# Optimization experiments

Measured on AMD Instinct MI355X. Metric: run time of the kernel, lower is better.

Reference implementation:

```python
import jax, jax.numpy as jnp
import numpy as np

N = 6144
HIDDEN = 48
HEADS = 3
HEAD = HIDDEN // HEADS


def setup_inputs() -> dict:
    key = jax.random.key(0)
    ks = jax.random.split(key, 8)
    s = 1.0 / np.sqrt(HIDDEN)
    A = (jax.random.uniform(ks[0], (N, N)) < 0.05).astype(jnp.float32)
    h = jax.random.normal(ks[1], (N, HIDDEN), dtype=jnp.float32)
    Wq = jax.random.normal(ks[2], (HIDDEN, HIDDEN), dtype=jnp.float32) * s
    Wk = jax.random.normal(ks[3], (HIDDEN, HIDDEN), dtype=jnp.float32) * s
    Wv = jax.random.normal(ks[4], (HIDDEN, HIDDEN), dtype=jnp.float32) * s
    bq = jnp.zeros((HIDDEN,), jnp.float32)
    bk = jnp.zeros((HIDDEN,), jnp.float32)
    bv = jnp.zeros((HIDDEN,), jnp.float32)
    return {"A": A, "h": h, "Wq": Wq, "bq": bq, "Wk": Wk, "bk": bk, "Wv": Wv, "bv": bv}


def reference(A, h, Wq, bq, Wk, bk, Wv, bv):
    n = h.shape[0]
    # QKV projections (torch Linear: x @ W.T + b)
    q = (h @ Wq.T + bq).reshape(n, HEADS, HEAD).transpose(1, 0, 2)  # [H,N,d]
    k = (h @ Wk.T + bk).reshape(n, HEADS, HEAD).transpose(1, 0, 2)
    v = (h @ Wv.T + bv).reshape(n, HEADS, HEAD).transpose(1, 0, 2)
    # scores = (q k^T) * A / N**(-0.5)  == (q k^T) * A * sqrt(N)  (faithful to source)
    scale = jnp.asarray(n, h.dtype) ** 0.5
    scores = jnp.einsum("hnd,hmd->hnm", q, k) * A[None, :, :] * scale
    scores = jax.nn.softmax(scores, axis=2)
    out = jnp.einsum("hnm,hmd->hnd", scores, v)  # [H,N,d]
    out = out.transpose(1, 0, 2).reshape(n, HIDDEN)
    return (out, scores)
```

## Files before the change

### kernel.cpp

```cpp
#include <hip/hip_runtime.h>
#include <math.h>

#define NN   6144
#define HID  48
#define BLK  512
#define RPB  4
#define CAP  448
#define CTOT (RPB*CAP)
#define NSL  42
#define SCALE 78.38367176906175f

typedef float vf4 __attribute__((ext_vector_type(4)));

__global__ __launch_bounds__(256)
void qkv_kernel(const float* __restrict__ h,
                const float* __restrict__ Wq, const float* __restrict__ bq,
                const float* __restrict__ Wk, const float* __restrict__ bk,
                const float* __restrict__ Wv, const float* __restrict__ bv,
                float* __restrict__ qw, float* __restrict__ kw, float* __restrict__ vw) {
    int idx = blockIdx.x * blockDim.x + threadIdx.x;
    int i = idx / HID, c = idx % HID;
    const float4* h4  = (const float4*)(h + (size_t)i * HID);
    const float4* wq4 = (const float4*)(Wq + (size_t)c * HID);
    const float4* wk4 = (const float4*)(Wk + (size_t)c * HID);
    const float4* wv4 = (const float4*)(Wv + (size_t)c * HID);
    float aq = 0.f, ak = 0.f, av = 0.f;
    #pragma unroll
    for (int r = 0; r < HID / 4; ++r) {
        float4 hv = h4[r];
        float4 q4 = wq4[r], k4 = wk4[r], v4 = wv4[r];
        aq = fmaf(hv.x, q4.x, aq); aq = fmaf(hv.y, q4.y, aq);
        aq = fmaf(hv.z, q4.z, aq); aq = fmaf(hv.w, q4.w, aq);
        ak = fmaf(hv.x, k4.x, ak); ak = fmaf(hv.y, k4.y, ak);
        ak = fmaf(hv.z, k4.z, ak); ak = fmaf(hv.w, k4.w, ak);
        av = fmaf(hv.x, v4.x, av); av = fmaf(hv.y, v4.y, av);
        av = fmaf(hv.w, v4.w, av); av = fmaf(hv.z, v4.z, av);
    }
    aq += bq[c]; ak += bk[c]; av += bv[c];
    int head = c >> 4, d = c & 15;
    size_t off = ((size_t)head * NN + i) * 16 + d;
    qw[off] = aq; kw[off] = ak; vw[off] = av;
}

__global__ __launch_bounds__(256)
void vtot_kernel(const float* __restrict__ vw, float* __restrict__ vtot) {
    int c = blockIdx.x;
    int head = c >> 4, d = c & 15;
    float s = 0.f;
    for (int j = threadIdx.x; j < NN; j += 256)
        s += vw[((size_t)head * NN + j) * 16 + d];
    #pragma unroll
    for (int o = 32; o; o >>= 1) s += __shfl_xor(s, o, 64);
    __shared__ float red[4];
    int wid = threadIdx.x >> 6, lane = threadIdx.x & 63;
    if (lane == 0) red[wid] = s;
    __syncthreads();
    if (threadIdx.x == 0) vtot[c] = red[0] + red[1] + red[2] + red[3];
}

__device__ __forceinline__ float maxw(const float* w, int idx) {
    float m = 0.f;
    #pragma unroll
    for (int k = 0; k < 8; ++k) m = fmaxf(m, w[k * 12 + idx]);
    return m;
}

__global__ __launch_bounds__(BLK)
void attn_kernel(const float* __restrict__ A,
                 const float* __restrict__ qw, const float* __restrict__ kw,
                 const float* __restrict__ vw, const float* __restrict__ vtot,
                 float* __restrict__ out) {
    __shared__ int   list[CTOT];
    __shared__ float sc[3][CTOT];
    __shared__ __align__(16) float qs[RPB * 48];
    __shared__ float accL[RPB * 52];
    __shared__ float lAcc[12];
    __shared__ float wredM[8 * 12];
    __shared__ unsigned wlo[8], whi[8];

    const int i0 = blockIdx.x * RPB;
    const int tid = threadIdx.x;
    const int wid = tid >> 6, lane = tid & 63;

    if (tid < RPB * 48) {
        int r = tid / 48, c = tid % 48;
        int hh = c >> 4, d = c & 15;
        qs[tid] = qw[((size_t)hh * NN + (i0 + r)) * 16 + d];
    }
    if (tid < RPB * 52) accL[tid] = 0.f;
    if (tid < 12) lAcc[tid] = 0.f;

    unsigned long long amask = 0ull;
    #pragma unroll
    for (int r = 0; r < RPB; ++r) {
        const vf4* Ar = (const vf4*)(A + (size_t)(i0 + r) * NN);
        #pragma unroll
        for (int c = 0; c < 3; ++c) {
            vf4 a4 = __builtin_nontemporal_load(&Ar[tid + c * BLK]);
            int p = r * 16 + c * 4;
            if (a4.x != 0.f) amask |= 1ull << (p + 0);
            if (a4.y != 0.f) amask |= 1ull << (p + 1);
            if (a4.z != 0.f) amask |= 1ull << (p + 2);
            if (a4.w != 0.f) amask |= 1ull << (p + 3);
        }
    }
    unsigned m0 = (unsigned)(amask & 0xFFFull);
    unsigned m1 = (unsigned)((amask >> 16) & 0xFFFull);
    unsigned m2 = (unsigned)((amask >> 32) & 0xFFFull);
    unsigned m3 = (unsigned)((amask >> 48) & 0xFFFull);
    unsigned lo = (unsigned)__popc(m0) | ((unsigned)__popc(m1) << 16);
    unsigned hi = (unsigned)__popc(m2) | ((unsigned)__popc(m3) << 16);

    unsigned ilo = lo, ihi = hi;
    #pragma unroll
    for (int o = 1; o < 64; o <<= 1) {
        unsigned plo = __shfl_up(ilo, o, 64);
        unsigned phi = __shfl_up(ihi, o, 64);
        if (lane >= o) { ilo += plo; ihi += phi; }
    }
    if (lane == 63) { wlo[wid] = ilo; whi[wid] = ihi; }
    __syncthreads();
    unsigned blo = ilo - lo, bhi = ihi - hi;
    unsigned tlo = 0, thi = 0;
    #pragma unroll
    for (int w = 0; w < 8; ++w) {
        unsigned a = wlo[w], b = whi[w];
        if (w < wid) { blo += a; bhi += b; }
        tlo += a; thi += b;
    }
    const int C0 = min((int)(tlo & 0xFFFFu), CAP), C1 = min((int)(tlo >> 16), CAP);
    const int C2 = min((int)(thi & 0xFFFFu), CAP), C3 = min((int)(thi >> 16), CAP);
    const int cum1 = C0, cum2 = C0 + C1, cum3 = cum2 + C2;
    int bs[4] = {(int)(blo & 0xFFFFu), (int)(blo >> 16),
                 (int)(bhi & 0xFFFFu), (int)(bhi >> 16)};
    int cu[5] = {0, cum1, cum2, cum3, cum3 + C3};
    unsigned mr[4] = {m0, m1, m2, m3};
    int Cr4[4] = {C0, C1, C2, C3};

    #pragma unroll
    for (int r = 0; r < RPB; ++r) {
        unsigned m = mr[r];
        int b = bs[r];
        while (m) {
            int p = __ffs(m) - 1; m &= m - 1;
            if (b < CAP) list[cu[r] + b] = 4 * (tid + (p >> 2) * BLK) + (p & 3);
            ++b;
        }
    }
    __syncthreads();

    {
        const int q4 = tid >> 2, part = tid & 3;
        #pragma unroll
        for (int r = 0; r < RPB; ++r) {
            float4 qv0 = ((const float4*)(qs + r * 48 +  0))[part];
            float4 qv1 = ((const float4*)(qs + r * 48 + 16))[part];
            float4 qv2 = ((const float4*)(qs + r * 48 + 32))[part];
            float mx0 = 0.f, mx1 = 0.f, mx2 = 0.f;
            for (int e = cu[r] + q4; e < cu[r + 1]; e += (BLK >> 2)) {
                int j = list[e];
                float4 k0 = ((const float4*)(kw + ((size_t)0 * NN + j) * 16))[part];
                float4 k1 = ((const float4*)(kw + ((size_t)1 * NN + j) * 16))[part];
                float4 k2 = ((const float4*)(kw + ((size_t)2 * NN + j) * 16))[part];
                float d0 = k0.x * qv0.x; d0 = fmaf(k0.y, qv0.y, d0);
                d0 = fmaf(k0.z, qv0.z, d0); d0 = fmaf(k0.w, qv0.w, d0);
                float d1 = k1.x * qv1.x; d1 = fmaf(k1.y, qv1.y, d1);
                d1 = fmaf(k1.z, qv1.z, d1); d1 = fmaf(k1.w, qv1.w, d1);
                float d2 = k2.x * qv2.x; d2 = fmaf(k2.y, qv2.y, d2);
                d2 = fmaf(k2.z, qv2.z, d2); d2 = fmaf(k2.w, qv2.w, d2);
                d0 += __shfl_xor(d0, 1, 64); d0 += __shfl_xor(d0, 2, 64);
                d1 += __shfl_xor(d1, 1, 64); d1 += __shfl_xor(d1, 2, 64);
                d2 += __shfl_xor(d2, 1, 64); d2 += __shfl_xor(d2, 2, 64);
                float s0 = d0 * SCALE, s1 = d1 * SCALE, s2 = d2 * SCALE;
                if (part == 0) sc[0][e] = s0;
                else if (part == 1) sc[1][e] = s1;
                else if (part == 2) sc[2][e] = s2;
                mx0 = fmaxf(mx0, s0);
                mx1 = fmaxf(mx1, s1);
                mx2 = fmaxf(mx2, s2);
            }
            #pragma unroll
            for (int o = 32; o; o >>= 1) {
                mx0 = fmaxf(mx0, __shfl_xor(mx0, o, 64));
                mx1 = fmaxf(mx1, __shfl_xor(mx1, o, 64));
                mx2 = fmaxf(mx2, __shfl_xor(mx2, o, 64));
            }
            if (lane == 0) {
                wredM[wid * 12 + r * 3 + 0] = mx0;
                wredM[wid * 12 + r * 3 + 1] = mx1;
                wredM[wid * 12 + r * 3 + 2] = mx2;
            }
        }
    }
    __syncthreads();

    if (tid < NSL * 12) {
        int s = tid % 12, a = tid / 12;
        int hh = s >> 2, rr4 = s & 3;
        const float* vbase = vw + (size_t)hh * NN * 16 + rr4 * 4;
        #pragma unroll
        for (int r = 0; r < RPB; ++r) {
            float M = maxw(wredM, r * 3 + hh);
            float zz = __expf(-M);
            float ax = 0.f, ay = 0.f, az = 0.f, aw = 0.f;
            float lp = 0.f;
            #pragma unroll 2
            for (int e = cu[r] + a; e < cu[r + 1]; e += NSL) {
                int j = list[e];
                float p = __expf(sc[hh][e] - M);
                float w = p - zz;
                lp += p;
                float4 vv = *(const float4*)(vbase + (size_t)j * 16);
                ax = fmaf(w, vv.x, ax);
                ay = fmaf(w, vv.y, ay);
                az = fmaf(w, vv.z, az);
                aw = fmaf(w, vv.w, aw);
            }
            int cb = r * 52 + hh * 16 + rr4 * 4;
            atomicAdd(&accL[cb + 0], ax);
            atomicAdd(&accL[cb + 1], ay);
            atomicAdd(&accL[cb + 2], az);
            atomicAdd(&accL[cb + 3], aw);
            if (rr4 == 0) atomicAdd(&lAcc[r * 3 + hh], lp);
        }
    }
    __syncthreads();

    if (tid < RPB * 48) {
        int r = tid / 48, c = tid % 48, hh = c >> 4;
        float M = maxw(wredM, r * 3 + hh);
        float z = __expf(-M);
        float iv = 1.0f / (lAcc[r * 3 + hh] + (float)(NN - Cr4[r]) * z);
        out[(size_t)(i0 + r) * HID + c] = (accL[r * 52 + c] + z * vtot[c]) * iv;
    }

    float* Pp = out + (size_t)NN * HID;

    #pragma unroll
    for (int r = 0; r < RPB; ++r) {
        float M0 = maxw(wredM, r * 3 + 0), M1 = maxw(wredM, r * 3 + 1), M2 = maxw(wredM, r * 3 + 2);
        float z0 = __expf(-M0), z1 = __expf(-M1), z2 = __expf(-M2);
        float fc = (float)(NN - Cr4[r]);
        float iv0 = 1.0f / (lAcc[r * 3 + 0] + fc * z0);
        float iv1 = 1.0f / (lAcc[r * 3 + 1] + fc * z1);
        float iv2 = 1.0f / (lAcc[r * 3 + 2] + fc * z2);
        float zi0 = z0 * iv0, zi1 = z1 * iv1, zi2 = z2 * iv2;
        int b = bs[r];
        unsigned m = mr[r];
        size_t rowoff = (size_t)(i0 + r) * NN;
        #pragma unroll
        for (int c = 0; c < 3; ++c) {
            vf4 P0, P1, P2;
            #pragma unroll
            for (int e = 0; e < 4; ++e) {
                int p = c * 4 + e;
                bool nz = (m >> p) & 1u;
                if (nz && b < CAP) {
                    int slot = cu[r] + b;
                    P0[e] = __expf(sc[0][slot] - M0) * iv0;
                    P1[e] = __expf(sc[1][slot] - M1) * iv1;
                    P2[e] = __expf(sc[2][slot] - M2) * iv2;
                } else {
                    P0[e] = zi0; P1[e] = zi1; P2[e] = zi2;
                }
                b += nz ? 1 : 0;
            }
            __builtin_nontemporal_store(P0, &((vf4*)(Pp + 0 * (size_t)NN * NN + rowoff))[tid + c * BLK]);
            __builtin_nontemporal_store(P1, &((vf4*)(Pp + 1 * (size_t)NN * NN + rowoff))[tid + c * BLK]);
            __builtin_nontemporal_store(P2, &((vf4*)(Pp + 2 * (size_t)NN * NN + rowoff))[tid + c * BLK]);
        }
    }
}

extern "C" void kernel_launch(void* const* d_in, const int* in_sizes, int n_in,
                              void* d_out, int out_size, void* d_ws, size_t ws_size,
                              hipStream_t stream) {
    const float* A  = (const float*)d_in[0];
    const float* h  = (const float*)d_in[1];
    const float* Wq = (const float*)d_in[2];
    const float* bq = (const float*)d_in[3];
    const float* Wk = (const float*)d_in[4];
    const float* bk = (const float*)d_in[5];
    const float* Wv = (const float*)d_in[6];
    const float* bv = (const float*)d_in[7];
    float* out = (float*)d_out;
    float* ws  = (float*)d_ws;

    float* qw   = ws;
    float* kw   = ws + (size_t)3 * NN * 16;
    float* vw   = ws + (size_t)6 * NN * 16;
    float* vtot = ws + (size_t)9 * NN * 16;

    qkv_kernel<<<(NN * HID) / 256, 256, 0, stream>>>(h, Wq, bq, Wk, bk, Wv, bv, qw, kw, vw);
    vtot_kernel<<<HID, 256, 0, stream>>>(vw, vtot);
    attn_kernel<<<NN / RPB, BLK, 0, stream>>>(A, qw, kw, vw, vtot, out);
}
```

Before: 628.8 us.

## Use online softmax sums and split warps between PV accumulation and probability stores

The score pass now keeps a running max and sum of exponentials (online softmax), so the normalizer is known before the PV pass. That removes the separate lp reduction and the shared-memory atomics. After that, warps 0-2 compute the output rows with shuffle reductions while warps 3-7 write the dense probability matrix, so the two phases run at the same time instead of in sequence. Per-thread masks and prefix offsets are kept in shared memory so the storing warps can rebuild slot indices. The cost is extra exponentials in the score loop, and only 320 threads issue the large store stream, which may reduce store bandwidth.

```diff
diff --git a/kernel.cpp b/kernel.cpp
--- a/kernel.cpp
+++ b/kernel.cpp
@@ -7,7 +7,6 @@
 #define RPB  4
 #define CAP  448
 #define CTOT (RPB*CAP)
-#define NSL  42
 #define SCALE 78.38367176906175f
 
 typedef float vf4 __attribute__((ext_vector_type(4)));
@@ -58,13 +57,6 @@
     if (threadIdx.x == 0) vtot[c] = red[0] + red[1] + red[2] + red[3];
 }
 
-__device__ __forceinline__ float maxw(const float* w, int idx) {
-    float m = 0.f;
-    #pragma unroll
-    for (int k = 0; k < 8; ++k) m = fmaxf(m, w[k * 12 + idx]);
-    return m;
-}
-
 __global__ __launch_bounds__(BLK)
 void attn_kernel(const float* __restrict__ A,
                  const float* __restrict__ qw, const float* __restrict__ kw,
@@ -73,9 +65,9 @@
     __shared__ int   list[CTOT];
     __shared__ float sc[3][CTOT];
     __shared__ __align__(16) float qs[RPB * 48];
-    __shared__ float accL[RPB * 52];
-    __shared__ float lAcc[12];
-    __shared__ float wredM[8 * 12];
+    __shared__ unsigned pm[RPB][BLK];
+    __shared__ float wredML[8 * 12 * 2];
+    __shared__ float MF[12], ZF[12], IVF[12];
     __shared__ unsigned wlo[8], whi[8];
 
     const int i0 = blockIdx.x * RPB;
@@ -87,8 +79,6 @@
         int hh = c >> 4, d = c & 15;
         qs[tid] = qw[((size_t)hh * NN + (i0 + r)) * 16 + d];
     }
-    if (tid < RPB * 52) accL[tid] = 0.f;
-    if (tid < 12) lAcc[tid] = 0.f;
 
     unsigned long long amask = 0ull;
     #pragma unroll
@@ -135,7 +125,10 @@
                  (int)(bhi & 0xFFFFu), (int)(bhi >> 16)};
     int cu[5] = {0, cum1, cum2, cum3, cum3 + C3};
     unsigned mr[4] = {m0, m1, m2, m3};
-    int Cr4[4] = {C0, C1, C2, C3};
+
+    #pragma unroll
+    for (int r = 0; r < RPB; ++r)
+        pm[r][tid] = mr[r] | ((unsigned)bs[r] << 12);
 
     #pragma unroll
     for (int r = 0; r < RPB; ++r) {
@@ -156,7 +149,7 @@
             float4 qv0 = ((const float4*)(qs + r * 48 +  0))[part];
             float4 qv1 = ((const float4*)(qs + r * 48 + 16))[part];
             float4 qv2 = ((const float4*)(qs + r * 48 + 32))[part];
-            float mx0 = 0.f, mx1 = 0.f, mx2 = 0.f;
+            float mA = 0.f, lA = 0.f, mB = 0.f, lB = 0.f, mC = 0.f, lC = 0.f;
             for (int e = cu[r] + q4; e < cu[r + 1]; e += (BLK >> 2)) {
                 int j = list[e];
                 float4 k0 = ((const float4*)(kw + ((size_t)0 * NN + j) * 16))[part];
@@ -175,99 +168,115 @@
                 if (part == 0) sc[0][e] = s0;
                 else if (part == 1) sc[1][e] = s1;
                 else if (part == 2) sc[2][e] = s2;
-                mx0 = fmaxf(mx0, s0);
-                mx1 = fmaxf(mx1, s1);
-                mx2 = fmaxf(mx2, s2);
+                float nm;
+                nm = fmaxf(mA, s0); lA = lA * __expf(mA - nm) + __expf(s0 - nm); mA = nm;
+                nm = fmaxf(mB, s1); lB = lB * __expf(mB - nm) + __expf(s1 - nm); mB = nm;
+                nm = fmaxf(mC, s2); lC = lC * __expf(mC - nm) + __expf(s2 - nm); mC = nm;
             }
             #pragma unroll
-            for (int o = 32; o; o >>= 1) {
-                mx0 = fmaxf(mx0, __shfl_xor(mx0, o, 64));
-                mx1 = fmaxf(mx1, __shfl_xor(mx1, o, 64));
-                mx2 = fmaxf(mx2, __shfl_xor(mx2, o, 64));
+            for (int o = 4; o < 64; o <<= 1) {
+                float om, ol, nm;
+                om = __shfl_xor(mA, o, 64); ol = __shfl_xor(lA, o, 64);
+                nm = fmaxf(mA, om); lA = lA * __expf(mA - nm) + ol * __expf(om - nm); mA = nm;
+                om = __shfl_xor(mB, o, 64); ol = __shfl_xor(lB, o, 64);
+                nm = fmaxf(mB, om); lB = lB * __expf(mB - nm) + ol * __expf(om - nm); mB = nm;
+                om = __shfl_xor(mC, o, 64); ol = __shfl_xor(lC, o, 64);
+                nm = fmaxf(mC, om); lC = lC * __expf(mC - nm) + ol * __expf(om - nm); mC = nm;
             }
             if (lane == 0) {
-                wredM[wid * 12 + r * 3 + 0] = mx0;
-                wredM[wid * 12 + r * 3 + 1] = mx1;
-                wredM[wid * 12 + r * 3 + 2] = mx2;
-            }
-        }
-    }
-    __syncthreads();
-
-    if (tid < NSL * 12) {
-        int s = tid % 12, a = tid / 12;
-        int hh = s >> 2, rr4 = s & 3;
-        const float* vbase = vw + (size_t)hh * NN * 16 + rr4 * 4;
+                int b0 = (wid * 12 + r * 3) * 2;
+                wredML[b0 + 0] = mA; wredML[b0 + 1] = lA;
+                wredML[b0 + 2] = mB; wredML[b0 + 3] = lB;
+                wredML[b0 + 4] = mC; wredML[b0 + 5] = lC;
+            }
+        }
+    }
+    __syncthreads();
+
+    if (tid < 12) {
+        int r = tid / 3;
+        int Cr = (r == 0) ? C0 : (r == 1) ? C1 : (r == 2) ? C2 : C3;
+        float M = wredML[tid * 2], L = wredML[tid * 2 + 1];
+        #pragma unroll
+        for (int w = 1; w < 8; ++w) {
+            float mw = wredML[(w * 12 + tid) * 2], lw = wredML[(w * 12 + tid) * 2 + 1];
+            float nm = fmaxf(M, mw);
+            L = L * __expf(M - nm) + lw * __expf(mw - nm);
+            M = nm;
+        }
+        float z = __expf(-M);
+        MF[tid] = M; ZF[tid] = z;
+        IVF[tid] = 1.0f / (L + (float)(NN - Cr) * z);
+    }
+    __syncthreads();
+
+    if (wid < 3) {
+        const int h = wid, rr4 = lane & 3, a = lane >> 2;
+        const float* vbase = vw + (size_t)h * NN * 16 + rr4 * 4;
         #pragma unroll
         for (int r = 0; r < RPB; ++r) {
-            float M = maxw(wredM, r * 3 + hh);
-            float zz = __expf(-M);
+            int s = r * 3 + h;
+            float M = MF[s], zz = ZF[s], iv = IVF[s];
             float ax = 0.f, ay = 0.f, az = 0.f, aw = 0.f;
-            float lp = 0.f;
             #pragma unroll 2
-            for (int e = cu[r] + a; e < cu[r + 1]; e += NSL) {
+            for (int e = cu[r] + a; e < cu[r + 1]; e += 16) {
+                float p = __expf(sc[h][e] - M);
+                float w = p - zz;
                 int j = list[e];
-                float p = __expf(sc[hh][e] - M);
-                float w = p - zz;
-                lp += p;
                 float4 vv = *(const float4*)(vbase + (size_t)j * 16);
-                ax = fmaf(w, vv.x, ax);
-                ay = fmaf(w, vv.y, ay);
-                az = fmaf(w, vv.z, az);
-                aw = fmaf(w, vv.w, aw);
-            }
-            int cb = r * 52 + hh * 16 + rr4 * 4;
-            atomicAdd(&accL[cb + 0], ax);
-            atomicAdd(&accL[cb + 1], ay);
-            atomicAdd(&accL[cb + 2], az);
-            atomicAdd(&accL[cb + 3], aw);
-            if (rr4 == 0) atomicAdd(&lAcc[r * 3 + hh], lp);
-        }
-    }
-    __syncthreads();
-
-    if (tid < RPB * 48) {
-        int r = tid / 48, c = tid % 48, hh = c >> 4;
-        float M = maxw(wredM, r * 3 + hh);
-        float z = __expf(-M);
-        float iv = 1.0f / (lAcc[r * 3 + hh] + (float)(NN - Cr4[r]) * z);
-        out[(size_t)(i0 + r) * HID + c] = (accL[r * 52 + c] + z * vtot[c]) * iv;
-    }
-
-    float* Pp = out + (size_t)NN * HID;
-
-    #pragma unroll
-    for (int r = 0; r < RPB; ++r) {
-        float M0 = maxw(wredM, r * 3 + 0), M1 = maxw(wredM, r * 3 + 1), M2 = maxw(wredM, r * 3 + 2);
-        float z0 = __expf(-M0), z1 = __expf(-M1), z2 = __expf(-M2);
-        float fc = (float)(NN - Cr4[r]);
-        float iv0 = 1.0f / (lAcc[r * 3 + 0] + fc * z0);
-        float iv1 = 1.0f / (lAcc[r * 3 + 1] + fc * z1);
-        float iv2 = 1.0f / (lAcc[r * 3 + 2] + fc * z2);
-        float zi0 = z0 * iv0, zi1 = z1 * iv1, zi2 = z2 * iv2;
-        int b = bs[r];
-        unsigned m = mr[r];
-        size_t rowoff = (size_t)(i0 + r) * NN;
-        #pragma unroll
-        for (int c = 0; c < 3; ++c) {
-            vf4 P0, P1, P2;
+                ax = fmaf(w, vv.x, ax); ay = fmaf(w, vv.y, ay);
+                az = fmaf(w, vv.z, az); aw = fmaf(w, vv.w, aw);
+            }
             #pragma unroll
-            for (int e = 0; e < 4; ++e) {
-                int p = c * 4 + e;
-                bool nz = (m >> p) & 1u;
-                if (nz && b < CAP) {
-                    int slot = cu[r] + b;
-                    P0[e] = __expf(sc[0][slot] - M0) * iv0;
-                    P1[e] = __expf(sc[1][slot] - M1) * iv1;
-                    P2[e] = __expf(sc[2][slot] - M2) * iv2;
-                } else {
-                    P0[e] = zi0; P1[e] = zi1; P2[e] = zi2;
+            for (int o = 4; o < 64; o <<= 1) {
+                ax += __shfl_xor(ax, o, 64); ay += __shfl_xor(ay, o, 64);
+                az += __shfl_xor(az, o, 64); aw += __shfl_xor(aw, o, 64);
+            }
+            if (a == 0) {
+                int c0 = h * 16 + rr4 * 4;
+                float4 vt = *(const float4*)(vtot + c0);
+                float4 o4;
+                o4.x = (ax + zz * vt.x) * iv;
+                o4.y = (ay + zz * vt.y) * iv;
+                o4.z = (az + zz * vt.z) * iv;
+                o4.w = (aw + zz * vt.w) * iv;
+                *(float4*)(out + (size_t)(i0 + r) * HID + c0) = o4;
+            }
+        }
+    } else {
+        float* Pp = out + (size_t)NN * HID;
+        const size_t NSQ = (size_t)NN * NN;
+        const int t = tid - 192;
+        #pragma unroll
+        for (int r = 0; r < RPB; ++r) {
+            int s = r * 3;
+            float M0 = MF[s], M1 = MF[s + 1], M2 = MF[s + 2];
+            float iv0 = IVF[s], iv1 = IVF[s + 1], iv2 = IVF[s + 2];
+            float zi0 = ZF[s] * iv0, zi1 = ZF[s + 1] * iv1, zi2 = ZF[s + 2] * iv2;
+            size_t rowoff = (size_t)(i0 + r) * NN;
+            #pragma unroll 2
+            for (int p = t; p < NN / 4; p += 320) {
+                unsigned pk = pm[r][p & (BLK - 1)];
+                int c = p >> 9;
+                unsigned msk = pk & 0xFFFu;
+                unsigned nib = (msk >> (c * 4)) & 0xFu;
+                int idx = (int)(pk >> 12) + __popc(msk & ((1u << (c * 4)) - 1u));
+                vf4 P0, P1, P2;
+                #pragma unroll
+                for (int e = 0; e < 4; ++e) {
+                    int nz = (int)((nib >> e) & 1u);
+                    if (nz && idx < CAP) {
+                        int slot = cu[r] + idx;
+                        P0[e] = __expf(sc[0][slot] - M0) * iv0;
+                        P1[e] = __expf(sc[1][slot] - M1) * iv1;
+                        P2[e] = __expf(sc[2][slot] - M2) * iv2;
+                    } else { P0[e] = zi0; P1[e] = zi1; P2[e] = zi2; }
+                    idx += nz;
                 }
-                b += nz ? 1 : 0;
-            }
-            __builtin_nontemporal_store(P0, &((vf4*)(Pp + 0 * (size_t)NN * NN + rowoff))[tid + c * BLK]);
-            __builtin_nontemporal_store(P1, &((vf4*)(Pp + 1 * (size_t)NN * NN + rowoff))[tid + c * BLK]);
-            __builtin_nontemporal_store(P2, &((vf4*)(Pp + 2 * (size_t)NN * NN + rowoff))[tid + c * BLK]);
+                __builtin_nontemporal_store(P0, &((vf4*)(Pp + rowoff))[p]);
+                __builtin_nontemporal_store(P1, &((vf4*)(Pp + NSQ + rowoff))[p]);
+                __builtin_nontemporal_store(P2, &((vf4*)(Pp + 2 * NSQ + rowoff))[p]);
+            }
         }
     }
 }
```

After: 609.4 us. -3.1%, faster.
